# Kernel tuning notes

Measured on AMD Instinct MI355X. Metric: run time of the kernel, lower is better.

The kernel has to match this reference:

```python
import jax, jax.numpy as jnp
import numpy as np

N_NODES = 100000
N_EDGES = 1600000
NFEAT, NHID, NCLASS = 128, 64, 16


def setup_inputs() -> dict:
    key = jax.random.key(0)
    ks = jax.random.split(key, 6)
    x = jax.random.normal(ks[0], (N_NODES, NFEAT), dtype=jnp.float32)
    src = jax.random.randint(ks[1], (N_EDGES,), 0, N_NODES)
    dst = jax.random.randint(ks[2], (N_EDGES,), 0, N_NODES)
    # Glorot-ish init for the two GraphConv weights, zero bias (DGL default)
    W1 = jax.random.normal(ks[3], (NFEAT, NHID), dtype=jnp.float32) * (1.0 / np.sqrt(NFEAT))
    b1 = jnp.zeros((NHID,), dtype=jnp.float32)
    W2 = jax.random.normal(ks[4], (NHID, NCLASS), dtype=jnp.float32) * (1.0 / np.sqrt(NHID))
    b2 = jnp.zeros((NCLASS,), dtype=jnp.float32)
    return {"x": x, "src": src, "dst": dst, "W1": W1, "b1": b1, "W2": W2, "b2": b2}


def _graph_conv(h, W, b, src, dst, norm_src, norm_dst, n_nodes):
    """DGL GraphConv with norm='both': D_out^{-1/2} A D_in^{-1/2} h W + b.
    Apply W before aggregation when it reduces dimensionality (DGL's in>out path);
    the math is identical either way."""
    if W.shape[0] > W.shape[1]:
        h = h @ W
    h = h * norm_src[:, None]                                   # scale source feats
    agg = jax.ops.segment_sum(h[src], dst, num_segments=n_nodes)  # sparse A @ h
    agg = agg * norm_dst[:, None]
    if W.shape[0] <= W.shape[1]:
        agg = agg @ W
    return agg + b


def reference(x, src, dst, W1, b1, W2, b2):
    n = x.shape[0]
    ones = jnp.ones(src.shape, dtype=x.dtype)
    out_deg = jax.ops.segment_sum(ones, src, num_segments=n)
    in_deg = jax.ops.segment_sum(ones, dst, num_segments=n)
    norm_src = jnp.maximum(out_deg, 1.0) ** -0.5  # degree clamp as in DGL
    norm_dst = jnp.maximum(in_deg, 1.0) ** -0.5
    h = jax.nn.relu(_graph_conv(x, W1, b1, src, dst, norm_src, norm_dst, n))
    # dropout: p=0 / eval mode -> identity
    h = _graph_conv(h, W2, b2, src, dst, norm_src, norm_dst, n)
    return jax.nn.log_softmax(h, axis=1)
```

## Files before the change

kernel.cpp:

```cpp
#include <hip/hip_runtime.h>
#include <hip/hip_bf16.h>

#define NN 100000
#define NE 1600000
#define NF 128
#define NH 64
#define NC 16
#define NB1 391
#define GBIN 256
#define CHUNK 6250
#define BBUK 196
#define NCB 196
#define NGRP 1563

typedef __attribute__((ext_vector_type(8))) short short8v;
typedef __attribute__((ext_vector_type(4))) float float4v;

__device__ __forceinline__ float us2f(unsigned short u) {
    return __uint_as_float(((unsigned int)u) << 16);
}
__device__ __forceinline__ float bflo(unsigned u) {
    return __uint_as_float(u << 16);
}
__device__ __forceinline__ float bfhi(unsigned u) {
    return __uint_as_float(u & 0xFFFF0000u);
}
__device__ __forceinline__ unsigned short f2us_rn(float f) {
    unsigned int u = __float_as_uint(f);
    return (unsigned short)((u + 0x7FFFu + ((u >> 16) & 1u)) >> 16);
}
__device__ __forceinline__ float ldf(const void* p, size_t i, bool f32) {
    return f32 ? ((const float*)p)[i] : us2f(((const unsigned short*)p)[i]);
}

__global__ void k_sniff(const unsigned short* __restrict__ xu, int* __restrict__ mode) {
    __shared__ int cnt;
    if (threadIdx.x == 0) cnt = 0;
    __syncthreads();
    int c = 0;
    for (int i = threadIdx.x; i < 4096; i += 256) {
        unsigned int e = (xu[i] >> 7) & 0xFFu;
        if (e >= 160u) c++;
    }
    atomicAdd(&cnt, c);
    __syncthreads();
    if (threadIdx.x == 0) mode[0] = (cnt >= 16) ? 1 : 0;
}

__global__ void k_deg(const int4* __restrict__ src4, const int4* __restrict__ dst4,
                      int* __restrict__ deg_out, int* __restrict__ deg_in) {
    int i = blockIdx.x * blockDim.x + threadIdx.x;
    if (i < NE / 4) {
        int4 s = src4[i], d = dst4[i];
        atomicAdd(&deg_out[s.x], 1); atomicAdd(&deg_out[s.y], 1);
        atomicAdd(&deg_out[s.z], 1); atomicAdd(&deg_out[s.w], 1);
        atomicAdd(&deg_in[d.x], 1);  atomicAdd(&deg_in[d.y], 1);
        atomicAdd(&deg_in[d.z], 1);  atomicAdd(&deg_in[d.w], 1);
    }
}

__global__ void k_scatter(const int* __restrict__ src, const int* __restrict__ dst,
                          int* __restrict__ cursor, int* __restrict__ srcs_sorted) {
    int e = blockIdx.x * blockDim.x + threadIdx.x;
    if (e < NE) {
        int p = atomicAdd(&cursor[dst[e]], 1);
        srcs_sorted[p] = src[e];
    }
}

__global__ void k_scan_a(const int* __restrict__ deg_in, int* __restrict__ bsum) {
    __shared__ int s[256];
    int i = blockIdx.x * 256 + threadIdx.x;
    s[threadIdx.x] = (i < NN) ? deg_in[i] : 0;
    __syncthreads();
    for (int off = 128; off > 0; off >>= 1) {
        if (threadIdx.x < off) s[threadIdx.x] += s[threadIdx.x + off];
        __syncthreads();
    }
    if (threadIdx.x == 0) bsum[blockIdx.x] = s[0];
}

__global__ void k_scan_b(const int* __restrict__ bsum, int* __restrict__ boff) {
    __shared__ int s[512];
    int t = threadIdx.x;
    s[t] = (t < NB1) ? bsum[t] : 0;
    __syncthreads();
    for (int off = 1; off < 512; off <<= 1) {
        int v = (t >= off) ? s[t - off] : 0;
        __syncthreads();
        s[t] += v;
        __syncthreads();
    }
    if (t < NB1) boff[t] = (t == 0) ? 0 : s[t - 1];
}

__global__ void k_scan_c(const int* __restrict__ deg_in, const int* __restrict__ deg_out,
                         const int* __restrict__ boff, int* __restrict__ row_off,
                         int* __restrict__ cursor, float* __restrict__ nsrc,
                         float* __restrict__ ndst) {
    __shared__ int s[256];
    int t = threadIdx.x;
    int i = blockIdx.x * 256 + t;
    int d = (i < NN) ? deg_in[i] : 0;
    s[t] = d;
    __syncthreads();
    for (int off = 1; off < 256; off <<= 1) {
        int v = (t >= off) ? s[t - off] : 0;
        __syncthreads();
        s[t] += v;
        __syncthreads();
    }
    int excl = s[t] - d + boff[blockIdx.x];
    if (i < NN) {
        row_off[i] = excl;
        cursor[i]  = excl;
        ndst[i] = rsqrtf(fmaxf((float)d, 1.0f));
        nsrc[i] = rsqrtf(fmaxf((float)deg_out[i], 1.0f));
        if (i == NN - 1) row_off[NN] = excl + d;
    }
}

__global__ __launch_bounds__(256) void k_hist2(const int* __restrict__ src,
                                               const int* __restrict__ dst,
                                               int* __restrict__ counts_d,
                                               int* __restrict__ counts_s) {
    __shared__ int hd[BBUK], hs[BBUK];
    for (int i = threadIdx.x; i < BBUK; i += 256) { hd[i] = 0; hs[i] = 0; }
    __syncthreads();
    const int g = blockIdx.x;
    const int e0 = g * CHUNK;
    for (int i = threadIdx.x; i < CHUNK; i += 256) {
        atomicAdd(&hd[dst[e0 + i] >> 9], 1);
        atomicAdd(&hs[src[e0 + i] >> 9], 1);
    }
    __syncthreads();
    for (int i = threadIdx.x; i < BBUK; i += 256) {
        counts_d[i * GBIN + g] = hd[i];
        counts_s[i * GBIN + g] = hs[i];
    }
}

__global__ void k_cs_a(const int* __restrict__ counts, int* __restrict__ csum) {
    __shared__ int s[256];
    int i = blockIdx.x * 256 + threadIdx.x;
    s[threadIdx.x] = counts[i];
    __syncthreads();
    for (int off = 128; off > 0; off >>= 1) {
        if (threadIdx.x < off) s[threadIdx.x] += s[threadIdx.x + off];
        __syncthreads();
    }
    if (threadIdx.x == 0) csum[blockIdx.x] = s[0];
}

__global__ void k_cs_b2(const int* __restrict__ csum, int* __restrict__ coff) {
    __shared__ int s[512];
    int t = threadIdx.x;
    int half = t >> 8, j = t & 255;
    s[t] = (j < NCB) ? csum[half * NCB + j] : 0;
    __syncthreads();
    for (int off = 1; off < 256; off <<= 1) {
        int v = (j >= off) ? s[t - off] : 0;
        __syncthreads();
        s[t] += v;
        __syncthreads();
    }
    if (j < NCB) coff[half * NCB + j] = (j == 0) ? 0 : s[t - 1];
}

__global__ void k_cs_c(int* __restrict__ counts, const int* __restrict__ coff) {
    __shared__ int s[256];
    int t = threadIdx.x;
    int i = blockIdx.x * 256 + t;
    int v = counts[i];
    s[t] = v;
    __syncthreads();
    for (int off = 1; off < 256; off <<= 1) {
        int u = (t >= off) ? s[t - off] : 0;
        __syncthreads();
        s[t] += u;
        __syncthreads();
    }
    counts[i] = s[t] - v + coff[blockIdx.x];
}

__global__ __launch_bounds__(256) void k_binscatter2(const int* __restrict__ src,
                                                     const int* __restrict__ dst,
                                                     const int* __restrict__ counts_d,
                                                     const int* __restrict__ counts_s,
                                                     unsigned int* __restrict__ packed,
                                                     unsigned short* __restrict__ packed2) {
    __shared__ int curd[BBUK], curs[BBUK];
    const int g = blockIdx.x;
    for (int i = threadIdx.x; i < BBUK; i += 256) {
        curd[i] = counts_d[i * GBIN + g];
        curs[i] = counts_s[i * GBIN + g];
    }
    __syncthreads();
    const int e0 = g * CHUNK;
    for (int i = threadIdx.x; i < CHUNK; i += 256) {
        int s = src[e0 + i], d = dst[e0 + i];
        int pd = atomicAdd(&curd[d >> 9], 1);
        packed[pd] = ((unsigned)s << 9) | (unsigned)(d & 511);
        int ps = atomicAdd(&curs[s >> 9], 1);
        packed2[ps] = (unsigned short)(s & 511);
    }
}

__global__ __launch_bounds__(256) void k_bdeg_out_nsrc(const int* __restrict__ counts_s,
                                                       const unsigned short* __restrict__ packed2,
                                                       float* __restrict__ nsrc) {
    __shared__ int h[512];
    const int b = blockIdx.x;
    const int n0 = b << 9;
    const int nlim = (NN - n0 < 512) ? (NN - n0) : 512;
    for (int j = threadIdx.x; j < 512; j += 256) h[j] = 0;
    __syncthreads();
    const int beg = counts_s[b * GBIN];
    const int end = (b + 1 < BBUK) ? counts_s[(b + 1) * GBIN] : NE;
    for (int i = beg + threadIdx.x; i < end; i += 256)
        atomicAdd(&h[packed2[i] & 511u], 1);
    __syncthreads();
    for (int j = threadIdx.x; j < nlim; j += 256)
        nsrc[n0 + j] = rsqrtf(fmaxf((float)h[j], 1.0f));
}

__global__ __launch_bounds__(256) void k_bucket_all(const int* __restrict__ counts_d,
                                                    const unsigned int* __restrict__ packed,
                                                    int* __restrict__ row_off,
                                                    float* __restrict__ ndst,
                                                    int* __restrict__ srcs_sorted) {
    __shared__ int h[512];
    const int b = blockIdx.x;
    const int n0 = b << 9;
    const int nlim = (NN - n0 < 512) ? (NN - n0) : 512;
    const int t = threadIdx.x;
    for (int j = t; j < 512; j += 256) h[j] = 0;
    __syncthreads();
    const int beg = counts_d[b * GBIN];
    const int end = (b + 1 < BBUK) ? counts_d[(b + 1) * GBIN] : NE;
    for (int i = beg + t; i < end; i += 256)
        atomicAdd(&h[packed[i] & 511u], 1);
    __syncthreads();
    const int degA = h[t], degB = h[t + 256];
    int offset = 1;
    #pragma unroll
    for (int d = 256; d > 0; d >>= 1) {
        __syncthreads();
        if (t < d) {
            int ai = offset * (2 * t + 1) - 1;
            int bi = offset * (2 * t + 2) - 1;
            h[bi] += h[ai];
        }
        offset <<= 1;
    }
    __syncthreads();
    if (t == 0) h[511] = 0;
    #pragma unroll
    for (int d = 1; d < 512; d <<= 1) {
        offset >>= 1;
        __syncthreads();
        if (t < d) {
            int ai = offset * (2 * t + 1) - 1;
            int bi = offset * (2 * t + 2) - 1;
            int tmp = h[ai]; h[ai] = h[bi]; h[bi] += tmp;
        }
    }
    __syncthreads();
    const int r0 = beg + h[t];
    const int r1 = beg + h[t + 256];
    if (t < nlim) {
        row_off[n0 + t] = r0;
        ndst[n0 + t] = rsqrtf(fmaxf((float)degA, 1.0f));
    }
    if (t + 256 < nlim) {
        row_off[n0 + t + 256] = r1;
        ndst[n0 + t + 256] = rsqrtf(fmaxf((float)degB, 1.0f));
    }
    if (n0 + nlim == NN && t == 0) row_off[NN] = end;
    __syncthreads();
    h[t] = r0; h[t + 256] = r1;
    __syncthreads();
    for (int i = beg + t; i < end; i += 256) {
        unsigned v = packed[i];
        int p = atomicAdd(&h[v & 511u], 1);
        srcs_sorted[p] = (int)(v >> 9);
    }
}

__global__ void k_prepW(const void* __restrict__ W1, unsigned short* __restrict__ W1f,
                        const int* __restrict__ mode) {
    const bool f32 = (mode[0] != 0);
    for (int i = threadIdx.x; i < 1024; i += 256) {
        const int kcnt = i >> 6, lane = i & 63;
        const int kc = kcnt >> 2, nt = kcnt & 3;
        const int quad = lane >> 4, col = lane & 15;
        #pragma unroll
        for (int j = 0; j < 8; ++j) {
            const size_t idx = (size_t)(kc * 32 + quad * 8 + j) * NH + nt * 16 + col;
            W1f[(size_t)i * 8 + j] = f32 ? f2us_rn(((const float*)W1)[idx])
                                         : ((const unsigned short*)W1)[idx];
        }
    }
}

__global__ __launch_bounds__(256) void k_gemm1_mfma(
    const void* __restrict__ x, const unsigned short* __restrict__ W1f,
    const float* __restrict__ nsrc, unsigned short* __restrict__ h1,
    const int* __restrict__ mode)
{
    const bool f32 = (mode[0] != 0);
    const int tid = threadIdx.x;
    const int wave = tid >> 6, lane = tid & 63;
    const int col = lane & 15, quad = lane >> 4;

    short8v bfrag[16];
    #pragma unroll
    for (int f = 0; f < 16; ++f)
        bfrag[f] = *(const short8v*)(W1f + ((size_t)f * 64 + lane) * 8);

    const int base = blockIdx.x * 64 + wave * 16;
    int arow = base + col;
    if (arow > NN - 1) arow = NN - 1;

    short8v afrag[4];
    if (f32) {
        const float4* ap = (const float4*)((const float*)x + (size_t)arow * NF);
        #pragma unroll
        for (int kc = 0; kc < 4; ++kc) {
            float4 v0 = ap[kc * 8 + quad * 2];
            float4 v1 = ap[kc * 8 + quad * 2 + 1];
            short8v af;
            af[0] = (short)f2us_rn(v0.x); af[1] = (short)f2us_rn(v0.y);
            af[2] = (short)f2us_rn(v0.z); af[3] = (short)f2us_rn(v0.w);
            af[4] = (short)f2us_rn(v1.x); af[5] = (short)f2us_rn(v1.y);
            af[6] = (short)f2us_rn(v1.z); af[7] = (short)f2us_rn(v1.w);
            afrag[kc] = af;
        }
    } else {
        const uint4* ap = (const uint4*)((const unsigned short*)x + (size_t)arow * NF);
        #pragma unroll
        for (int kc = 0; kc < 4; ++kc) {
            uint4 v = ap[kc * 4 + quad];
            afrag[kc] = *reinterpret_cast<const short8v*>(&v);
        }
    }

    float4v acc[4];
    #pragma unroll
    for (int nt = 0; nt < 4; ++nt) acc[nt] = (float4v){0.f, 0.f, 0.f, 0.f};
    #pragma unroll
    for (int kc = 0; kc < 4; ++kc)
        #pragma unroll
        for (int nt = 0; nt < 4; ++nt)
            acc[nt] = __builtin_amdgcn_mfma_f32_16x16x32_bf16(afrag[kc], bfrag[kc * 4 + nt], acc[nt], 0, 0, 0);

    #pragma unroll
    for (int reg = 0; reg < 4; ++reg) {
        const int row = base + quad * 4 + reg;
        if (row < NN) {
            const float ns = nsrc[row];
            unsigned short* hp = h1 + (size_t)row * NH + col;
            hp[0]  = f2us_rn(acc[0][reg] * ns);
            hp[16] = f2us_rn(acc[1][reg] * ns);
            hp[32] = f2us_rn(acc[2][reg] * ns);
            hp[48] = f2us_rn(acc[3][reg] * ns);
        }
    }
}

__global__ __launch_bounds__(256) void k_agg1csr(
    const int* __restrict__ row_off, const int* __restrict__ srcs,
    const unsigned short* __restrict__ h1, const float* __restrict__ ndst,
    const float* __restrict__ nsrc, const void* __restrict__ b1,
    const void* __restrict__ W2, const int* __restrict__ mode,
    unsigned short* __restrict__ h2)
{
    const bool f32 = (mode[0] != 0);
    const int lane = threadIdx.x & 63;
    const int q  = lane >> 4;
    const int li = lane & 15;

    const float bias0 = ldf(b1, 4*li+0, f32), bias1 = ldf(b1, 4*li+1, f32);
    const float bias2 = ldf(b1, 4*li+2, f32), bias3 = ldf(b1, 4*li+3, f32);
    float w2[4][4];
    #pragma unroll
    for (int j = 0; j < 4; ++j)
        #pragma unroll
        for (int m = 0; m < 4; ++m)
            w2[j][m] = ldf(W2, (size_t)(4*li+j)*NC + (q + 4*m), f32);

    const int wid = (blockIdx.x * blockDim.x + threadIdx.x) >> 6;
    const int nw  = (gridDim.x * blockDim.x) >> 6;
    const uint2* __restrict__ h1v = (const uint2*)h1;
    const unsigned uli = (unsigned)li;

    int row = wid;
    if (row >= NN) return;
    int beg = row_off[row];
    int end = row_off[row + 1];
    float nd = ndst[row];
    float ns = nsrc[row];

    while (row < NN) {
        const int nrow = row + nw;
        int nbeg = 0, nend = 0;
        float nnd = 0.f, nns = 0.f;
        if (nrow < NN) {
            nbeg = row_off[nrow];
            nend = row_off[nrow + 1];
            nnd  = ndst[nrow];
            nns  = nsrc[nrow];
        }

        float ax = 0.f, ay = 0.f, az = 0.f, aw = 0.f;
        float bx = 0.f, by = 0.f, bz = 0.f, bw = 0.f;
        const int e1 = end - 1;
        int i = beg + q;
        while (i < end) {
            const int j1 = i + 4, j2 = i + 8, j3 = i + 12;
            const int t1 = (j1 < end) ? j1 : e1;
            const int t2 = (j2 < end) ? j2 : e1;
            const int t3 = (j3 < end) ? j3 : e1;
            const int s0 = srcs[(unsigned)i];
            const int s1 = srcs[(unsigned)t1];
            const int s2 = srcs[(unsigned)t2];
            const int s3 = srcs[(unsigned)t3];
            const uint2 v0 = h1v[(unsigned)s0 * 16u + uli];
            const uint2 v1 = h1v[(unsigned)s1 * 16u + uli];
            const uint2 v2 = h1v[(unsigned)s2 * 16u + uli];
            const uint2 v3 = h1v[(unsigned)s3 * 16u + uli];
            ax += bflo(v0.x); ay += bfhi(v0.x);
            az += bflo(v0.y); aw += bfhi(v0.y);
            if (j1 < end) {
                bx += bflo(v1.x); by += bfhi(v1.x);
                bz += bflo(v1.y); bw += bfhi(v1.y);
            }
            if (j2 < end) {
                ax += bflo(v2.x); ay += bfhi(v2.x);
                az += bflo(v2.y); aw += bfhi(v2.y);
            }
            if (j3 < end) {
                bx += bflo(v3.x); by += bfhi(v3.x);
                bz += bflo(v3.y); bw += bfhi(v3.y);
            }
            i += 16;
        }
        ax += bx; ay += by; az += bz; aw += bw;
        ax += __shfl_xor(ax, 16); ay += __shfl_xor(ay, 16);
        az += __shfl_xor(az, 16); aw += __shfl_xor(aw, 16);
        ax += __shfl_xor(ax, 32); ay += __shfl_xor(ay, 32);
        az += __shfl_xor(az, 32); aw += __shfl_xor(aw, 32);

        const float t0 = fmaxf(fmaf(ax, nd, bias0), 0.f);
        const float t1f = fmaxf(fmaf(ay, nd, bias1), 0.f);
        const float t2f = fmaxf(fmaf(az, nd, bias2), 0.f);
        const float t3f = fmaxf(fmaf(aw, nd, bias3), 0.f);

        float p0 = fmaf(t0,w2[0][0],fmaf(t1f,w2[1][0],fmaf(t2f,w2[2][0],t3f*w2[3][0])));
        float p1 = fmaf(t0,w2[0][1],fmaf(t1f,w2[1][1],fmaf(t2f,w2[2][1],t3f*w2[3][1])));
        float p2 = fmaf(t0,w2[0][2],fmaf(t1f,w2[1][2],fmaf(t2f,w2[2][2],t3f*w2[3][2])));
        float p3 = fmaf(t0,w2[0][3],fmaf(t1f,w2[1][3],fmaf(t2f,w2[2][3],t3f*w2[3][3])));
        #pragma unroll
        for (int off = 1; off <= 8; off <<= 1) {
            p0 += __shfl_xor(p0, off);
            p1 += __shfl_xor(p1, off);
            p2 += __shfl_xor(p2, off);
            p3 += __shfl_xor(p3, off);
        }
        if (li < 4) {
            float v = (li == 0) ? p0 : (li == 1) ? p1 : (li == 2) ? p2 : p3;
            h2[(size_t)row * NC + q + 4*li] = f2us_rn(v * ns);
        }

        row = nrow; beg = nbeg; end = nend; nd = nnd; ns = nns;
    }
}

__global__ __launch_bounds__(256) void k_out(
    const int* __restrict__ row_off, const int* __restrict__ srcs,
    const unsigned short* __restrict__ h2, const float* __restrict__ ndst,
    const void* __restrict__ b2, const int* __restrict__ mode,
    void* __restrict__ out)
{
    const bool f32 = (mode[0] != 0);
    const int lane = threadIdx.x & 63;
    const int q  = lane >> 3;
    const int li = lane & 7;
    const float b2v0 = ldf(b2, 2*li,   f32);
    const float b2v1 = ldf(b2, 2*li+1, f32);

    const int wid = (blockIdx.x * blockDim.x + threadIdx.x) >> 6;
    const int nw  = (gridDim.x * blockDim.x) >> 6;
    const unsigned* __restrict__ h2v = (const unsigned*)h2;
    const unsigned uli = (unsigned)li;

    int row = wid;
    if (row >= NN) return;
    int beg = row_off[row];
    int end = row_off[row + 1];
    float nd = ndst[row];

    while (row < NN) {
        const int nrow = row + nw;
        int nbeg = 0, nend = 0;
        float nnd = 0.f;
        if (nrow < NN) {
            nbeg = row_off[nrow];
            nend = row_off[nrow + 1];
            nnd  = ndst[nrow];
        }

        float a0 = 0.f, a1 = 0.f, c0 = 0.f, c1 = 0.f;
        const int e1 = end - 1;
        int i = beg + q;
        while (i < end) {
            const int j1 = i + 8;
            const int t1 = (j1 < end) ? j1 : e1;
            const int s0 = srcs[(unsigned)i];
            const int s1 = srcs[(unsigned)t1];
            const unsigned u0 = h2v[(unsigned)s0 * 8u + uli];
            const unsigned u1 = h2v[(unsigned)s1 * 8u + uli];
            a0 += bflo(u0); a1 += bfhi(u0);
            if (j1 < end) {
                c0 += bflo(u1); c1 += bfhi(u1);
            }
            i += 16;
        }
        a0 += c0; a1 += c1;
        #pragma unroll
        for (int off = 8; off <= 32; off <<= 1) {
            a0 += __shfl_xor(a0, off);
            a1 += __shfl_xor(a1, off);
        }
        float v0 = fmaf(a0, nd, b2v0);
        float v1 = fmaf(a1, nd, b2v1);
        float m = fmaxf(v0, v1);
        #pragma unroll
        for (int off = 1; off <= 4; off <<= 1) m = fmaxf(m, __shfl_xor(m, off));
        float sm = __expf(v0 - m) + __expf(v1 - m);
        #pragma unroll
        for (int off = 1; off <= 4; off <<= 1) sm += __shfl_xor(sm, off);
        const float lsm = __logf(sm);
        const float r0 = v0 - m - lsm, r1 = v1 - m - lsm;
        if (q == 0) {
            if (f32) {
                float2 o; o.x = r0; o.y = r1;
                *(float2*)((float*)out + (size_t)row * NC + 2*li) = o;
            } else {
                unsigned o = ((unsigned)f2us_rn(r1) << 16) | (unsigned)f2us_rn(r0);
                *(unsigned*)((unsigned short*)out + (size_t)row * NC + 2*li) = o;
            }
        }

        row = nrow; beg = nbeg; end = nend; nd = nnd;
    }
}

extern "C" void kernel_launch(void* const* d_in, const int* in_sizes, int n_in,
                              void* d_out, int out_size, void* d_ws, size_t ws_size,
                              hipStream_t stream) {
    const void* x  = d_in[0];
    const int* src = (const int*)d_in[1];
    const int* dst = (const int*)d_in[2];
    const void* W1 = d_in[3];
    const void* b1 = d_in[4];
    const void* W2 = d_in[5];
    const void* b2 = d_in[6];

    char* ws = (char*)d_ws;
    const size_t O_MODE = 0;
    const size_t O_W1F  = 1024;
    const size_t O_CNT  = O_W1F + 16384;
    const size_t O_CS   = O_CNT  + 401408;
    const size_t O_DEG  = O_CS   + 4096;
    const size_t O_NSRC = O_DEG  + 800000;
    const size_t O_NDST = O_NSRC + 400000;
    const size_t O_ROW  = O_NDST + 400000;
    const size_t O_CUR  = O_ROW  + 400128;
    const size_t O_BS   = O_CUR  + 400128;
    const size_t O_SRCS = O_BS   + 4096;
    const size_t O_H2   = O_SRCS + 6400000;
    const size_t O_H1   = O_H2   + 3200000;
    const size_t NEED = O_H1 + 12800000;
    const bool fast_csr = ws_size >= NEED;

    int*   mode     = (int*)(ws + O_MODE);
    unsigned short* W1f = (unsigned short*)(ws + O_W1F);
    int*   counts_d = (int*)(ws + O_CNT);
    int*   counts_s = counts_d + BBUK * GBIN;
    int*   csum     = (int*)(ws + O_CS);
    int*   coff     = (int*)(ws + O_CS + 2048);
    int*   deg_out  = (int*)(ws + O_DEG);
    int*   deg_in   = deg_out + NN;
    float* nsrc     = (float*)(ws + O_NSRC);
    float* ndst     = (float*)(ws + O_NDST);
    int*   row_off  = (int*)(ws + O_ROW);
    int*   cursor   = (int*)(ws + O_CUR);
    int*   bsum     = (int*)(ws + O_BS);
    int*   boff     = (int*)(ws + O_BS + 2048);
    int*   srcs_s   = (int*)(ws + O_SRCS);
    unsigned short* h2 = (unsigned short*)(ws + O_H2);
    unsigned short* h1 = (unsigned short*)(ws + O_H1);
    unsigned int*   packed  = (unsigned int*)(ws + O_H1);
    unsigned short* packed2 = (unsigned short*)(ws + O_H1 + 6400000);

    k_sniff<<<1, 256, 0, stream>>>((const unsigned short*)x, mode);
    k_prepW<<<1, 256, 0, stream>>>(W1, W1f, mode);
    if (fast_csr) {
        k_hist2<<<GBIN, 256, 0, stream>>>(src, dst, counts_d, counts_s);
        k_cs_a<<<2 * NCB, 256, 0, stream>>>(counts_d, csum);
        k_cs_b2<<<1, 512, 0, stream>>>(csum, coff);
        k_cs_c<<<2 * NCB, 256, 0, stream>>>(counts_d, coff);
        k_binscatter2<<<GBIN, 256, 0, stream>>>(src, dst, counts_d, counts_s, packed, packed2);
        k_bdeg_out_nsrc<<<BBUK, 256, 0, stream>>>(counts_s, packed2, nsrc);
        k_bucket_all<<<BBUK, 256, 0, stream>>>(counts_d, packed, row_off, ndst, srcs_s);
    } else {
        hipMemsetAsync(deg_out, 0, 2 * (size_t)NN * sizeof(int), stream);
        k_deg<<<(NE / 4 + 255) / 256, 256, 0, stream>>>((const int4*)src, (const int4*)dst, deg_out, deg_in);
        k_scan_a<<<NB1, 256, 0, stream>>>(deg_in, bsum);
        k_scan_b<<<1, 512, 0, stream>>>(bsum, boff);
        k_scan_c<<<NB1, 256, 0, stream>>>(deg_in, deg_out, boff, row_off, cursor, nsrc, ndst);
        k_scatter<<<(NE + 255) / 256, 256, 0, stream>>>(src, dst, cursor, srcs_s);
    }
    k_gemm1_mfma<<<NGRP, 256, 0, stream>>>(x, W1f, nsrc, h1, mode);
    k_agg1csr<<<2048, 256, 0, stream>>>(row_off, srcs_s, h1, ndst, nsrc, b1, W2, mode, h2);
    k_out<<<2048, 256, 0, stream>>>(row_off, srcs_s, h2, ndst, b2, mode, d_out);
}
```

Measured before the change: 277.6 us.

## Aggregate directly from dst-bucketed edges with LDS atomics, drop CSR build

Removes the per-bucket CSR construction kernel (prefix scan plus scatter into sorted source lists). Both aggregation layers now read the bucketed packed edges directly. Each 1024-thread block owns a half-bucket of 256 destination nodes and accumulates gathered features into shared-memory float atomics, then applies bias, ReLU, W2 (or log-softmax) in place. This saves a pass over the edges and the srcs_sorted writes, but trades ordered CSR row reads for heavy LDS atomic contention, and each block scans the whole bucket while keeping only half of it.

```diff
diff --git a/kernel.cpp b/kernel.cpp
--- a/kernel.cpp
+++ b/kernel.cpp
@@ -224,69 +224,6 @@
         nsrc[n0 + j] = rsqrtf(fmaxf((float)h[j], 1.0f));
 }
 
-__global__ __launch_bounds__(256) void k_bucket_all(const int* __restrict__ counts_d,
-                                                    const unsigned int* __restrict__ packed,
-                                                    int* __restrict__ row_off,
-                                                    float* __restrict__ ndst,
-                                                    int* __restrict__ srcs_sorted) {
-    __shared__ int h[512];
-    const int b = blockIdx.x;
-    const int n0 = b << 9;
-    const int nlim = (NN - n0 < 512) ? (NN - n0) : 512;
-    const int t = threadIdx.x;
-    for (int j = t; j < 512; j += 256) h[j] = 0;
-    __syncthreads();
-    const int beg = counts_d[b * GBIN];
-    const int end = (b + 1 < BBUK) ? counts_d[(b + 1) * GBIN] : NE;
-    for (int i = beg + t; i < end; i += 256)
-        atomicAdd(&h[packed[i] & 511u], 1);
-    __syncthreads();
-    const int degA = h[t], degB = h[t + 256];
-    int offset = 1;
-    #pragma unroll
-    for (int d = 256; d > 0; d >>= 1) {
-        __syncthreads();
-        if (t < d) {
-            int ai = offset * (2 * t + 1) - 1;
-            int bi = offset * (2 * t + 2) - 1;
-            h[bi] += h[ai];
-        }
-        offset <<= 1;
-    }
-    __syncthreads();
-    if (t == 0) h[511] = 0;
-    #pragma unroll
-    for (int d = 1; d < 512; d <<= 1) {
-        offset >>= 1;
-        __syncthreads();
-        if (t < d) {
-            int ai = offset * (2 * t + 1) - 1;
-            int bi = offset * (2 * t + 2) - 1;
-            int tmp = h[ai]; h[ai] = h[bi]; h[bi] += tmp;
-        }
-    }
-    __syncthreads();
-    const int r0 = beg + h[t];
-    const int r1 = beg + h[t + 256];
-    if (t < nlim) {
-        row_off[n0 + t] = r0;
-        ndst[n0 + t] = rsqrtf(fmaxf((float)degA, 1.0f));
-    }
-    if (t + 256 < nlim) {
-        row_off[n0 + t + 256] = r1;
-        ndst[n0 + t + 256] = rsqrtf(fmaxf((float)degB, 1.0f));
-    }
-    if (n0 + nlim == NN && t == 0) row_off[NN] = end;
-    __syncthreads();
-    h[t] = r0; h[t + 256] = r1;
-    __syncthreads();
-    for (int i = beg + t; i < end; i += 256) {
-        unsigned v = packed[i];
-        int p = atomicAdd(&h[v & 511u], 1);
-        srcs_sorted[p] = (int)(v >> 9);
-    }
-}
-
 __global__ void k_prepW(const void* __restrict__ W1, unsigned short* __restrict__ W1f,
                         const int* __restrict__ mode) {
     const bool f32 = (mode[0] != 0);
@@ -364,6 +301,191 @@
             hp[16] = f2us_rn(acc[1][reg] * ns);
             hp[32] = f2us_rn(acc[2][reg] * ns);
             hp[48] = f2us_rn(acc[3][reg] * ns);
+        }
+    }
+}
+
+__global__ __launch_bounds__(1024, 8) void k_aggbucket(
+    const int* __restrict__ counts_d, const unsigned int* __restrict__ packed,
+    const unsigned short* __restrict__ h1, const float* __restrict__ nsrc,
+    const void* __restrict__ b1, const void* __restrict__ W2,
+    const int* __restrict__ mode,
+    float* __restrict__ ndst, unsigned short* __restrict__ h2)
+{
+    __shared__ float acc[256][65];
+    __shared__ int   cnt[256];
+    __shared__ float w2l[1024];
+    __shared__ float b1l[64];
+
+    const int t = threadIdx.x;
+    const bool f32m = (mode[0] != 0);
+
+    float* af = &acc[0][0];
+    for (int j = t; j < 256 * 65; j += 1024) af[j] = 0.f;
+    if (t < 256) cnt[t] = 0;
+    w2l[t] = ldf(W2, t, f32m);
+    if (t < 64) b1l[t] = ldf(b1, t, f32m);
+    __syncthreads();
+
+    const int b    = blockIdx.x >> 1;
+    const int half = blockIdx.x & 1;
+    const int beg = counts_d[b * GBIN];
+    const int end = (b + 1 < BBUK) ? counts_d[(b + 1) * GBIN] : NE;
+
+    const int g  = t >> 4;
+    const int li = t & 15;
+    const uint2* __restrict__ h1v = (const uint2*)h1;
+    const int e1 = end - 1;
+
+    for (int i = beg + g; i < end; i += 128) {
+        const int ib = i + 64;
+        const unsigned wa = packed[(unsigned)i];
+        const unsigned wb = packed[(unsigned)((ib <= e1) ? ib : e1)];
+        const bool ma = (((wa >> 8) & 1u) == (unsigned)half);
+        const bool mb = (ib <= e1) && (((wb >> 8) & 1u) == (unsigned)half);
+        uint2 va, vb;
+        int dla = 0, dlb = 0;
+        if (ma) {
+            dla = (int)(wa & 255u);
+            va = h1v[(wa >> 9) * 16u + (unsigned)li];
+        }
+        if (mb) {
+            dlb = (int)(wb & 255u);
+            vb = h1v[(wb >> 9) * 16u + (unsigned)li];
+        }
+        if (ma) {
+            atomicAdd(&acc[dla][4 * li + 0], bflo(va.x));
+            atomicAdd(&acc[dla][4 * li + 1], bfhi(va.x));
+            atomicAdd(&acc[dla][4 * li + 2], bflo(va.y));
+            atomicAdd(&acc[dla][4 * li + 3], bfhi(va.y));
+            if (li == 0) atomicAdd(&cnt[dla], 1);
+        }
+        if (mb) {
+            atomicAdd(&acc[dlb][4 * li + 0], bflo(vb.x));
+            atomicAdd(&acc[dlb][4 * li + 1], bfhi(vb.x));
+            atomicAdd(&acc[dlb][4 * li + 2], bflo(vb.y));
+            atomicAdd(&acc[dlb][4 * li + 3], bfhi(vb.y));
+            if (li == 0) atomicAdd(&cnt[dlb], 1);
+        }
+    }
+    __syncthreads();
+
+    if (t < 512) {
+        const int nl = t >> 1;
+        const int ch = t & 1;
+        const int node = (b << 9) + (half << 8) + nl;
+        if (node < NN) {
+            const int deg = cnt[nl];
+            const float nd = rsqrtf(fmaxf((float)deg, 1.0f));
+            if (ch == 0) ndst[node] = nd;
+            const float ns = nsrc[node];
+            float p0 = 0.f, p1 = 0.f, p2 = 0.f, p3 = 0.f;
+            float p4 = 0.f, p5 = 0.f, p6 = 0.f, p7 = 0.f;
+            const int cb = ch * 8;
+            #pragma unroll 8
+            for (int f = 0; f < 64; ++f) {
+                const float tf = fmaxf(fmaf(acc[nl][f], nd, b1l[f]), 0.f);
+                const float* wr = &w2l[f * 16 + cb];
+                p0 = fmaf(tf, wr[0], p0); p1 = fmaf(tf, wr[1], p1);
+                p2 = fmaf(tf, wr[2], p2); p3 = fmaf(tf, wr[3], p3);
+                p4 = fmaf(tf, wr[4], p4); p5 = fmaf(tf, wr[5], p5);
+                p6 = fmaf(tf, wr[6], p6); p7 = fmaf(tf, wr[7], p7);
+            }
+            unsigned short* hp = h2 + (size_t)node * NC + cb;
+            hp[0] = f2us_rn(p0 * ns); hp[1] = f2us_rn(p1 * ns);
+            hp[2] = f2us_rn(p2 * ns); hp[3] = f2us_rn(p3 * ns);
+            hp[4] = f2us_rn(p4 * ns); hp[5] = f2us_rn(p5 * ns);
+            hp[6] = f2us_rn(p6 * ns); hp[7] = f2us_rn(p7 * ns);
+        }
+    }
+}
+
+__global__ __launch_bounds__(1024, 8) void k_outbucket(
+    const int* __restrict__ counts_d, const unsigned int* __restrict__ packed,
+    const unsigned short* __restrict__ h2, const float* __restrict__ ndst,
+    const void* __restrict__ b2, const int* __restrict__ mode,
+    void* __restrict__ out)
+{
+    __shared__ float acc2[256][17];
+    __shared__ float b2l[16];
+
+    const int t = threadIdx.x;
+    const bool f32m = (mode[0] != 0);
+
+    float* af = &acc2[0][0];
+    for (int j = t; j < 256 * 17; j += 1024) af[j] = 0.f;
+    if (t < 16) b2l[t] = ldf(b2, t, f32m);
+    __syncthreads();
+
+    const int b    = blockIdx.x >> 1;
+    const int half = blockIdx.x & 1;
+    const int beg = counts_d[b * GBIN];
+    const int end = (b + 1 < BBUK) ? counts_d[(b + 1) * GBIN] : NE;
+
+    const int g   = t >> 3;
+    const int li2 = t & 7;
+    const unsigned* __restrict__ h2v = (const unsigned*)h2;
+    const int e1 = end - 1;
+
+    for (int i = beg + g; i < end; i += 256) {
+        const int ib = i + 128;
+        const unsigned wa = packed[(unsigned)i];
+        const unsigned wb = packed[(unsigned)((ib <= e1) ? ib : e1)];
+        const bool ma = (((wa >> 8) & 1u) == (unsigned)half);
+        const bool mb = (ib <= e1) && (((wb >> 8) & 1u) == (unsigned)half);
+        unsigned ua, ub;
+        int dla = 0, dlb = 0;
+        if (ma) {
+            dla = (int)(wa & 255u);
+            ua = h2v[(wa >> 9) * 8u + (unsigned)li2];
+        }
+        if (mb) {
+            dlb = (int)(wb & 255u);
+            ub = h2v[(wb >> 9) * 8u + (unsigned)li2];
+        }
+        if (ma) {
+            atomicAdd(&acc2[dla][2 * li2 + 0], bflo(ua));
+            atomicAdd(&acc2[dla][2 * li2 + 1], bfhi(ua));
+        }
+        if (mb) {
+            atomicAdd(&acc2[dlb][2 * li2 + 0], bflo(ub));
+            atomicAdd(&acc2[dlb][2 * li2 + 1], bfhi(ub));
+        }
+    }
+    __syncthreads();
+
+    if (t < 256) {
+        const int node = (b << 9) + (half << 8) + t;
+        if (node < NN) {
+            const float nd = ndst[node];
+            float m = -3.4e38f;
+            #pragma unroll
+            for (int c = 0; c < 16; ++c)
+                m = fmaxf(m, fmaf(acc2[t][c], nd, b2l[c]));
+            float sm = 0.f;
+            #pragma unroll
+            for (int c = 0; c < 16; ++c)
+                sm += __expf(fmaf(acc2[t][c], nd, b2l[c]) - m);
+            const float lsm = __logf(sm);
+            if (f32m) {
+                float* op = (float*)out + (size_t)node * NC;
+                #pragma unroll
+                for (int c = 0; c < 16; c += 2) {
+                    float2 o;
+                    o.x = fmaf(acc2[t][c + 0], nd, b2l[c + 0]) - m - lsm;
+                    o.y = fmaf(acc2[t][c + 1], nd, b2l[c + 1]) - m - lsm;
+                    *(float2*)(op + c) = o;
+                }
+            } else {
+                unsigned short* op = (unsigned short*)out + (size_t)node * NC;
+                #pragma unroll
+                for (int c = 0; c < 16; c += 2) {
+                    const float r0 = fmaf(acc2[t][c + 0], nd, b2l[c + 0]) - m - lsm;
+                    const float r1 = fmaf(acc2[t][c + 1], nd, b2l[c + 1]) - m - lsm;
+                    *(unsigned*)(op + c) =
+                        ((unsigned)f2us_rn(r1) << 16) | (unsigned)f2us_rn(r0);
+                }
+            }
         }
     }
 }
@@ -601,8 +723,8 @@
     int*   srcs_s   = (int*)(ws + O_SRCS);
     unsigned short* h2 = (unsigned short*)(ws + O_H2);
     unsigned short* h1 = (unsigned short*)(ws + O_H1);
-    unsigned int*   packed  = (unsigned int*)(ws + O_H1);
-    unsigned short* packed2 = (unsigned short*)(ws + O_H1 + 6400000);
+    unsigned int*   packed  = (unsigned int*)(ws + O_SRCS);
+    unsigned short* packed2 = (unsigned short*)(ws + O_H1);
 
     k_sniff<<<1, 256, 0, stream>>>((const unsigned short*)x, mode);
     k_prepW<<<1, 256, 0, stream>>>(W1, W1f, mode);
@@ -613,7 +735,9 @@
         k_cs_c<<<2 * NCB, 256, 0, stream>>>(counts_d, coff);
         k_binscatter2<<<GBIN, 256, 0, stream>>>(src, dst, counts_d, counts_s, packed, packed2);
         k_bdeg_out_nsrc<<<BBUK, 256, 0, stream>>>(counts_s, packed2, nsrc);
-        k_bucket_all<<<BBUK, 256, 0, stream>>>(counts_d, packed, row_off, ndst, srcs_s);
+        k_gemm1_mfma<<<NGRP, 256, 0, stream>>>(x, W1f, nsrc, h1, mode);
+        k_aggbucket<<<2 * BBUK, 1024, 0, stream>>>(counts_d, packed, h1, nsrc, b1, W2, mode, ndst, h2);
+        k_outbucket<<<2 * BBUK, 1024, 0, stream>>>(counts_d, packed, h2, ndst, b2, mode, d_out);
     } else {
         hipMemsetAsync(deg_out, 0, 2 * (size_t)NN * sizeof(int), stream);
         k_deg<<<(NE / 4 + 255) / 256, 256, 0, stream>>>((const int4*)src, (const int4*)dst, deg_out, deg_in);
@@ -621,8 +745,8 @@
         k_scan_b<<<1, 512, 0, stream>>>(bsum, boff);
         k_scan_c<<<NB1, 256, 0, stream>>>(deg_in, deg_out, boff, row_off, cursor, nsrc, ndst);
         k_scatter<<<(NE + 255) / 256, 256, 0, stream>>>(src, dst, cursor, srcs_s);
-    }
-    k_gemm1_mfma<<<NGRP, 256, 0, stream>>>(x, W1f, nsrc, h1, mode);
-    k_agg1csr<<<2048, 256, 0, stream>>>(row_off, srcs_s, h1, ndst, nsrc, b1, W2, mode, h2);
-    k_out<<<2048, 256, 0, stream>>>(row_off, srcs_s, h2, ndst, b2, mode, d_out);
-}
+        k_gemm1_mfma<<<NGRP, 256, 0, stream>>>(x, W1f, nsrc, h1, mode);
+        k_agg1csr<<<2048, 256, 0, stream>>>(row_off, srcs_s, h1, ndst, nsrc, b1, W2, mode, h2);
+        k_out<<<2048, 256, 0, stream>>>(row_off, srcs_s, h2, ndst, b2, mode, d_out);
+    }
+}
```

New measurement: 1.045 ms. +276.3%, slower.
